# Kernel optimization log

Hardware: AMD Instinct MI355X
Metric: run time of the kernel (lower is better)

## Reference

```python
import jax, jax.numpy as jnp
import numpy as np

NUM_EXPERT = 16
IN_FEAT = 1024
OUT_FEAT = 2048
N_TOKENS = 4096


def setup_inputs() -> dict:
    key = jax.random.key(0)
    k1, k2, k3 = jax.random.split(key, 3)
    x = jax.random.uniform(k1, (N_TOKENS, IN_FEAT), dtype=jnp.float32)
    gate = jax.random.randint(k2, (N_TOKENS,), 0, NUM_EXPERT, dtype=jnp.int32)
    # expert weights: [num_expert, out_feat, in_feat]
    weight = jax.random.normal(k3, (NUM_EXPERT, OUT_FEAT, IN_FEAT), dtype=jnp.float32) * 0.02
    return {"x": x, "gate": gate, "weight": weight}


def reference(x, gate, weight):
    # out[b] = weight[gate[b]] @ x[b]
    # Avoid materializing weight[gate] ([B, O, I] would be huge): scan over the
    # small, fixed expert axis with input masking (tokens not routed to expert e
    # contribute zero rows to that expert's GEMM).
    B = x.shape[0]
    E, O, I = weight.shape
    out0 = jnp.zeros((B, O), dtype=x.dtype)

    def body(out, ew):
        e, W = ew  # W: [O, I]
        xm = jnp.where((gate == e)[:, None], x, 0.0)  # [B, I] masked tokens
        return out + jnp.einsum("bi,oi->bo", xm, W), None

    out, _ = jax.lax.scan(body, out0, (jnp.arange(E), weight))
    return out
```

## Files before the change

### kernel.cpp

```cpp
#include <hip/hip_runtime.h>
#include <hip/hip_bf16.h>
#include <stdint.h>

#define N_TOKENS   4096
#define IN_FEAT    1024
#define OUT_FEAT   2048
#define NUM_EXPERT 16

#define BM 128
#define BN 128
#define BK 32
#define NT (IN_FEAT / BK)
#define MAX_TILES 48
#define MAX_ROWS  6144

typedef __bf16 bf16x8 __attribute__((ext_vector_type(8)));
typedef float  f32x4  __attribute__((ext_vector_type(4)));
typedef unsigned short us8 __attribute__((ext_vector_type(8)));

__device__ __forceinline__ unsigned short f32_to_bf16_rne(float f) {
  union { float f; uint32_t u; } v; v.f = f;
  uint32_t u = v.u;
  u += 0x7fffu + ((u >> 16) & 1u);
  return (unsigned short)(u >> 16);
}

__device__ __forceinline__ void async_copy16(const void* g, void* l) {
  __builtin_amdgcn_global_load_lds(
      (const __attribute__((address_space(1))) unsigned int*)g,
      (__attribute__((address_space(3))) unsigned int*)l, 16, 0, 0);
}

__global__ void k_setup(const int* __restrict__ gate,
                        int* __restrict__ pstart,
                        int* __restrict__ tile_e,
                        int* __restrict__ tile_m,
                        int* __restrict__ row_token)
{
  __shared__ int cnt[NUM_EXPERT];
  __shared__ int cur[NUM_EXPERT];
  __shared__ int ps[NUM_EXPERT];
  const int tid = threadIdx.x;
  if (tid < NUM_EXPERT) { cnt[tid] = 0; cur[tid] = 0; }
  __syncthreads();
  for (int b = tid; b < N_TOKENS; b += 256) atomicAdd(&cnt[gate[b]], 1);
  for (int r = tid; r < MAX_ROWS; r += 256) row_token[r] = -1;
  __syncthreads();
  if (tid == 0) {
    int p = 0, tot = 0;
    for (int e = 0; e < NUM_EXPERT; ++e) {
      ps[e] = p; pstart[e] = p;
      int nt = (cnt[e] + BM - 1) / BM;
      for (int t = 0; t < nt; ++t) { tile_e[tot] = e; tile_m[tot] = t; ++tot; }
      p += nt * BM;
    }
    for (int s = tot; s < MAX_TILES; ++s) { tile_e[s] = -1; tile_m[s] = 0; }
  }
  __syncthreads();
  for (int b = tid; b < N_TOKENS; b += 256) {
    int e = gate[b];
    int pos = atomicAdd(&cur[e], 1);
    row_token[ps[e] + pos] = b;
  }
}

__global__ void k_gather_x(const float4* __restrict__ x,
                           const int* __restrict__ row_token,
                           us8* __restrict__ xs) {
  const int r = blockIdx.x * 2 + (threadIdx.x >> 7);
  const int c = threadIdx.x & 127;
  const int tok = row_token[r];
  us8 o;
  if (tok >= 0) {
    float4 a = x[tok * 256 + c * 2];
    float4 b = x[tok * 256 + c * 2 + 1];
    o[0] = f32_to_bf16_rne(a.x); o[1] = f32_to_bf16_rne(a.y);
    o[2] = f32_to_bf16_rne(a.z); o[3] = f32_to_bf16_rne(a.w);
    o[4] = f32_to_bf16_rne(b.x); o[5] = f32_to_bf16_rne(b.y);
    o[6] = f32_to_bf16_rne(b.z); o[7] = f32_to_bf16_rne(b.w);
  } else {
    o = (us8)0;
  }
  xs[r * 128 + c] = o;
}

__global__ void __launch_bounds__(256, 3)
k_gemm(const unsigned short* __restrict__ xs,
       const float* __restrict__ w,
       const int* __restrict__ pstart,
       const int* __restrict__ tile_e,
       const int* __restrict__ tile_m,
       const int* __restrict__ row_token,
       float* __restrict__ out) {
  __shared__ f32x4 Bs[2][1024];
  __shared__ int rowtok_s[BM];

  const int id  = blockIdx.y * 16 + blockIdx.x;
  const int r_  = id & 7;
  const int m_  = id >> 3;
  const int q3  = m_ % 3;
  const int n_  = m_ / 3;
  const int sub = n_ & 1;
  const int xt  = n_ >> 1;

  const int slot = 2 * (r_ + 8 * q3) + sub;
  const int e = tile_e[slot];
  if (e < 0) return;
  const int seg0 = pstart[e] + tile_m[slot] * BM;
  const int n0 = xt * BN;

  const int tid  = threadIdx.x;
  const int wid  = tid >> 6;
  const int lane = tid & 63;
  const int lr   = lane & 15;
  const int quad = lane >> 4;
  const int wm   = (wid >> 1) * 64;
  const int wn   = (wid & 1) * 64;

  if (tid < BM) rowtok_s[tid] = row_token[seg0 + tid];

  const int cB = (tid & 7) ^ ((tid >> 3) & 7);
  const float* bgp = w + (size_t)e * OUT_FEAT * IN_FEAT
                       + (size_t)(n0 + (tid >> 3)) * IN_FEAT + cB * 4;

  const unsigned short* ap =
      xs + (size_t)(seg0 + wm + lr) * IN_FEAT + quad * 8;

  f32x4 acc[4][4];
  const f32x4 z = {0.f, 0.f, 0.f, 0.f};
#pragma unroll
  for (int i = 0; i < 4; ++i)
#pragma unroll
    for (int j = 0; j < 4; ++j) acc[i][j] = z;

  auto stageB = [&](int t, int b) {
    const int k0 = t * BK;
    async_copy16(bgp + k0,                 Bs[b] + wid * 64);
    async_copy16(bgp + 32 * IN_FEAT + k0,  Bs[b] + 256 + wid * 64);
    async_copy16(bgp + 64 * IN_FEAT + k0,  Bs[b] + 512 + wid * 64);
    async_copy16(bgp + 96 * IN_FEAT + k0,  Bs[b] + 768 + wid * 64);
  };
  auto loadA = [&](int t, bf16x8* dst) {
#pragma unroll
    for (int mi = 0; mi < 4; ++mi)
      dst[mi] = *(const bf16x8*)(ap + (size_t)mi * 16 * IN_FEAT + t * BK);
  };

  bf16x8 afA[4], afB[4];

  stageB(0, 0);
  loadA(0, afA);

  asm volatile("s_waitcnt lgkmcnt(0)" ::: "memory");
  __builtin_amdgcn_s_barrier();

  auto step = [&](int t, bf16x8* afc, bf16x8* afn) {
    const int buf = t & 1;
    if (t + 1 < NT) {
      stageB(t + 1, buf ^ 1);
      loadA(t + 1, afn);
      asm volatile("s_waitcnt vmcnt(8)" ::: "memory");
    } else {
      asm volatile("s_waitcnt vmcnt(0)" ::: "memory");
    }
    __builtin_amdgcn_s_barrier();
    asm volatile("" ::: "memory");

    bf16x8 bf[4];
#pragma unroll
    for (int ni = 0; ni < 4; ++ni) {
      const int n = wn + ni * 16 + lr;
      f32x4 c0 = Bs[buf][n * 8 + ((2 * quad)     ^ (n & 7))];
      f32x4 c1 = Bs[buf][n * 8 + ((2 * quad + 1) ^ (n & 7))];
      bf16x8 b;
      b[0] = (__bf16)c0[0]; b[1] = (__bf16)c0[1];
      b[2] = (__bf16)c0[2]; b[3] = (__bf16)c0[3];
      b[4] = (__bf16)c1[0]; b[5] = (__bf16)c1[1];
      b[6] = (__bf16)c1[2]; b[7] = (__bf16)c1[3];
      bf[ni] = b;
    }
#pragma unroll
    for (int mi = 0; mi < 4; ++mi)
#pragma unroll
      for (int ni = 0; ni < 4; ++ni)
        acc[mi][ni] = __builtin_amdgcn_mfma_f32_16x16x32_bf16(
            afc[mi], bf[ni], acc[mi][ni], 0, 0, 0);

    asm volatile("" ::: "memory");
    __builtin_amdgcn_s_barrier();
  };

  for (int t = 0; t < NT; t += 2) {
    step(t,     afA, afB);
    step(t + 1, afB, afA);
  }

#pragma unroll
  for (int mi = 0; mi < 4; ++mi) {
    const int mb = wm + mi * 16 + quad * 4;
    const int t0 = rowtok_s[mb + 0];
    const int t1 = rowtok_s[mb + 1];
    const int t2 = rowtok_s[mb + 2];
    const int t3 = rowtok_s[mb + 3];
#pragma unroll
    for (int ni = 0; ni < 4; ++ni) {
      const int n = n0 + wn + ni * 16 + lr;
      f32x4 c = acc[mi][ni];
      if (t0 >= 0) out[(size_t)t0 * OUT_FEAT + n] = c[0];
      if (t1 >= 0) out[(size_t)t1 * OUT_FEAT + n] = c[1];
      if (t2 >= 0) out[(size_t)t2 * OUT_FEAT + n] = c[2];
      if (t3 >= 0) out[(size_t)t3 * OUT_FEAT + n] = c[3];
    }
  }
}

extern "C" void kernel_launch(void* const* d_in, const int* in_sizes, int n_in,
                              void* d_out, int out_size, void* d_ws, size_t ws_size,
                              hipStream_t stream) {
  const float* x    = (const float*)d_in[0];
  const int*   gate = (const int*)d_in[1];
  const float* w    = (const float*)d_in[2];
  float* out = (float*)d_out;

  char* ws = (char*)d_ws;
  unsigned short* xs = (unsigned short*)ws;
  int* row_token = (int*)(ws + 12582912);
  int* pstart = row_token + MAX_ROWS;
  int* tile_e = pstart + NUM_EXPERT;
  int* tile_m = tile_e + MAX_TILES;

  k_setup<<<1, 256, 0, stream>>>(gate, pstart, tile_e, tile_m, row_token);
  k_gather_x<<<MAX_ROWS / 2, 256, 0, stream>>>((const float4*)x, row_token,
                                               (us8*)xs);
  dim3 g(OUT_FEAT / BN, MAX_TILES);
  k_gemm<<<g, 256, 0, stream>>>(xs, w, pstart, tile_e, tile_m, row_token, out);
}
```

Measured before the change: 274.9 us.

## Assign one block per expert and N-window, looping over 512-row groups

Replaces the per-M-tile grid with a grid of (expert, 128-column window). Each 512-thread block covers up to 512 rows of an expert's segment per group, so each staged weight tile is reused across four times as many rows. The goal is to cut redundant fp32 weight loads from HBM, which dominate traffic. In exchange the grid shrinks to 256 blocks and per-wave accumulators double, which raises register pressure. Experts with more than 512 rows run the whole K loop again and reload the weights.

Result: faster. 260.4 us (-5.3%).

```diff
diff --git a/kernel.cpp b/kernel.cpp
--- a/kernel.cpp
+++ b/kernel.cpp
@@ -8,10 +8,10 @@
 #define NUM_EXPERT 16
 
 #define BM 128
-#define BN 128
 #define BK 32
 #define NT (IN_FEAT / BK)
-#define MAX_TILES 48
+#define BNW 128
+#define GROWS 512
 #define MAX_ROWS  6144
 
 typedef __bf16 bf16x8 __attribute__((ext_vector_type(8)));
@@ -33,8 +33,6 @@
 
 __global__ void k_setup(const int* __restrict__ gate,
                         int* __restrict__ pstart,
-                        int* __restrict__ tile_e,
-                        int* __restrict__ tile_m,
                         int* __restrict__ row_token)
 {
   __shared__ int cnt[NUM_EXPERT];
@@ -47,14 +45,12 @@
   for (int r = tid; r < MAX_ROWS; r += 256) row_token[r] = -1;
   __syncthreads();
   if (tid == 0) {
-    int p = 0, tot = 0;
+    int p = 0;
     for (int e = 0; e < NUM_EXPERT; ++e) {
       ps[e] = p; pstart[e] = p;
-      int nt = (cnt[e] + BM - 1) / BM;
-      for (int t = 0; t < nt; ++t) { tile_e[tot] = e; tile_m[tot] = t; ++tot; }
-      p += nt * BM;
-    }
-    for (int s = tot; s < MAX_TILES; ++s) { tile_e[s] = -1; tile_m[s] = 0; }
+      p += ((cnt[e] + BM - 1) / BM) * BM;
+    }
+    pstart[NUM_EXPERT] = p;
   }
   __syncthreads();
   for (int b = tid; b < N_TOKENS; b += 256) {
@@ -84,132 +80,134 @@
   xs[r * 128 + c] = o;
 }
 
-__global__ void __launch_bounds__(256, 3)
+__global__ void __launch_bounds__(512, 2)
 k_gemm(const unsigned short* __restrict__ xs,
        const float* __restrict__ w,
        const int* __restrict__ pstart,
-       const int* __restrict__ tile_e,
-       const int* __restrict__ tile_m,
        const int* __restrict__ row_token,
        float* __restrict__ out) {
   __shared__ f32x4 Bs[2][1024];
-  __shared__ int rowtok_s[BM];
-
-  const int id  = blockIdx.y * 16 + blockIdx.x;
-  const int r_  = id & 7;
-  const int m_  = id >> 3;
-  const int q3  = m_ % 3;
-  const int n_  = m_ / 3;
-  const int sub = n_ & 1;
-  const int xt  = n_ >> 1;
-
-  const int slot = 2 * (r_ + 8 * q3) + sub;
-  const int e = tile_e[slot];
-  if (e < 0) return;
-  const int seg0 = pstart[e] + tile_m[slot] * BM;
-  const int n0 = xt * BN;
+  __shared__ int rowtok_s[GROWS];
+
+  const int e    = blockIdx.x;
+  const int nwin = blockIdx.y * BNW;
+  const int seg0 = pstart[e];
+  const int seg_len = pstart[e + 1] - seg0;
+  if (seg_len <= 0) return;
 
   const int tid  = threadIdx.x;
   const int wid  = tid >> 6;
   const int lane = tid & 63;
   const int lr   = lane & 15;
   const int quad = lane >> 4;
-  const int wm   = (wid >> 1) * 64;
-  const int wn   = (wid & 1) * 64;
-
-  if (tid < BM) rowtok_s[tid] = row_token[seg0 + tid];
-
-  const int cB = (tid & 7) ^ ((tid >> 3) & 7);
+
+  const int rB = tid >> 3;
+  const int cB = (tid & 7) ^ (rB & 7);
   const float* bgp = w + (size_t)e * OUT_FEAT * IN_FEAT
-                       + (size_t)(n0 + (tid >> 3)) * IN_FEAT + cB * 4;
-
-  const unsigned short* ap =
-      xs + (size_t)(seg0 + wm + lr) * IN_FEAT + quad * 8;
-
-  f32x4 acc[4][4];
-  const f32x4 z = {0.f, 0.f, 0.f, 0.f};
-#pragma unroll
-  for (int i = 0; i < 4; ++i)
-#pragma unroll
-    for (int j = 0; j < 4; ++j) acc[i][j] = z;
+                       + (size_t)(nwin + rB) * IN_FEAT + cB * 4;
 
   auto stageB = [&](int t, int b) {
     const int k0 = t * BK;
-    async_copy16(bgp + k0,                 Bs[b] + wid * 64);
-    async_copy16(bgp + 32 * IN_FEAT + k0,  Bs[b] + 256 + wid * 64);
-    async_copy16(bgp + 64 * IN_FEAT + k0,  Bs[b] + 512 + wid * 64);
-    async_copy16(bgp + 96 * IN_FEAT + k0,  Bs[b] + 768 + wid * 64);
+    async_copy16(bgp + k0,                Bs[b] +       wid * 64);
+    async_copy16(bgp + 64 * IN_FEAT + k0, Bs[b] + 512 + wid * 64);
   };
-  auto loadA = [&](int t, bf16x8* dst) {
-#pragma unroll
-    for (int mi = 0; mi < 4; ++mi)
-      dst[mi] = *(const bf16x8*)(ap + (size_t)mi * 16 * IN_FEAT + t * BK);
-  };
-
-  bf16x8 afA[4], afB[4];
-
-  stageB(0, 0);
-  loadA(0, afA);
-
-  asm volatile("s_waitcnt lgkmcnt(0)" ::: "memory");
-  __builtin_amdgcn_s_barrier();
-
-  auto step = [&](int t, bf16x8* afc, bf16x8* afn) {
-    const int buf = t & 1;
-    if (t + 1 < NT) {
-      stageB(t + 1, buf ^ 1);
-      loadA(t + 1, afn);
-      asm volatile("s_waitcnt vmcnt(8)" ::: "memory");
-    } else {
-      asm volatile("s_waitcnt vmcnt(0)" ::: "memory");
-    }
+
+  const int nGroups = (seg_len + GROWS - 1) / GROWS;
+
+  for (int g = 0; g < nGroups; ++g) {
+    __syncthreads();
+
+    {
+      const int grow = g * GROWS + tid;
+      rowtok_s[tid] = (grow < seg_len) ? row_token[seg0 + grow] : -1;
+    }
+
+    const unsigned short* apm[4];
+#pragma unroll
+    for (int mi = 0; mi < 4; ++mi) {
+      const int grow = g * GROWS + wid * 64 + mi * 16 + lr;
+      const int arow = (grow < seg_len) ? grow : 0;
+      apm[mi] = xs + (size_t)(seg0 + arow) * IN_FEAT + quad * 8;
+    }
+
+    auto loadA = [&](int t, bf16x8* dst) {
+#pragma unroll
+      for (int mi = 0; mi < 4; ++mi)
+        dst[mi] = *(const bf16x8*)(apm[mi] + t * BK);
+    };
+
+    f32x4 acc[4][8];
+    const f32x4 z = {0.f, 0.f, 0.f, 0.f};
+#pragma unroll
+    for (int i = 0; i < 4; ++i)
+#pragma unroll
+      for (int j = 0; j < 8; ++j) acc[i][j] = z;
+
+    bf16x8 afA[4], afB[4];
+
+    stageB(0, 0);
+    loadA(0, afA);
+
+    asm volatile("s_waitcnt lgkmcnt(0)" ::: "memory");
     __builtin_amdgcn_s_barrier();
-    asm volatile("" ::: "memory");
-
-    bf16x8 bf[4];
-#pragma unroll
-    for (int ni = 0; ni < 4; ++ni) {
-      const int n = wn + ni * 16 + lr;
-      f32x4 c0 = Bs[buf][n * 8 + ((2 * quad)     ^ (n & 7))];
-      f32x4 c1 = Bs[buf][n * 8 + ((2 * quad + 1) ^ (n & 7))];
-      bf16x8 b;
-      b[0] = (__bf16)c0[0]; b[1] = (__bf16)c0[1];
-      b[2] = (__bf16)c0[2]; b[3] = (__bf16)c0[3];
-      b[4] = (__bf16)c1[0]; b[5] = (__bf16)c1[1];
-      b[6] = (__bf16)c1[2]; b[7] = (__bf16)c1[3];
-      bf[ni] = b;
-    }
-#pragma unroll
-    for (int mi = 0; mi < 4; ++mi)
-#pragma unroll
-      for (int ni = 0; ni < 4; ++ni)
-        acc[mi][ni] = __builtin_amdgcn_mfma_f32_16x16x32_bf16(
-            afc[mi], bf[ni], acc[mi][ni], 0, 0, 0);
-
-    asm volatile("" ::: "memory");
-    __builtin_amdgcn_s_barrier();
-  };
-
-  for (int t = 0; t < NT; t += 2) {
-    step(t,     afA, afB);
-    step(t + 1, afB, afA);
-  }
-
-#pragma unroll
-  for (int mi = 0; mi < 4; ++mi) {
-    const int mb = wm + mi * 16 + quad * 4;
-    const int t0 = rowtok_s[mb + 0];
-    const int t1 = rowtok_s[mb + 1];
-    const int t2 = rowtok_s[mb + 2];
-    const int t3 = rowtok_s[mb + 3];
-#pragma unroll
-    for (int ni = 0; ni < 4; ++ni) {
-      const int n = n0 + wn + ni * 16 + lr;
-      f32x4 c = acc[mi][ni];
-      if (t0 >= 0) out[(size_t)t0 * OUT_FEAT + n] = c[0];
-      if (t1 >= 0) out[(size_t)t1 * OUT_FEAT + n] = c[1];
-      if (t2 >= 0) out[(size_t)t2 * OUT_FEAT + n] = c[2];
-      if (t3 >= 0) out[(size_t)t3 * OUT_FEAT + n] = c[3];
+
+    auto step = [&](int t, bf16x8* afc, bf16x8* afn) {
+      const int buf = t & 1;
+      if (t + 1 < NT) {
+        stageB(t + 1, buf ^ 1);
+        loadA(t + 1, afn);
+        asm volatile("s_waitcnt vmcnt(6)" ::: "memory");
+      } else {
+        asm volatile("s_waitcnt vmcnt(0)" ::: "memory");
+      }
+      __builtin_amdgcn_s_barrier();
+      asm volatile("" ::: "memory");
+
+      bf16x8 bf[8];
+#pragma unroll
+      for (int ni = 0; ni < 8; ++ni) {
+        const int n = ni * 16 + lr;
+        f32x4 c0 = Bs[buf][n * 8 + ((2 * quad)     ^ (n & 7))];
+        f32x4 c1 = Bs[buf][n * 8 + ((2 * quad + 1) ^ (n & 7))];
+        bf16x8 b;
+        b[0] = (__bf16)c0[0]; b[1] = (__bf16)c0[1];
+        b[2] = (__bf16)c0[2]; b[3] = (__bf16)c0[3];
+        b[4] = (__bf16)c1[0]; b[5] = (__bf16)c1[1];
+        b[6] = (__bf16)c1[2]; b[7] = (__bf16)c1[3];
+        bf[ni] = b;
+      }
+#pragma unroll
+      for (int mi = 0; mi < 4; ++mi)
+#pragma unroll
+        for (int ni = 0; ni < 8; ++ni)
+          acc[mi][ni] = __builtin_amdgcn_mfma_f32_16x16x32_bf16(
+              afc[mi], bf[ni], acc[mi][ni], 0, 0, 0);
+
+      asm volatile("" ::: "memory");
+      __builtin_amdgcn_s_barrier();
+    };
+
+    for (int t = 0; t < NT; t += 2) {
+      step(t,     afA, afB);
+      step(t + 1, afB, afA);
+    }
+
+#pragma unroll
+    for (int mi = 0; mi < 4; ++mi) {
+      const int mb = wid * 64 + mi * 16 + quad * 4;
+      const int t0 = rowtok_s[mb + 0];
+      const int t1 = rowtok_s[mb + 1];
+      const int t2 = rowtok_s[mb + 2];
+      const int t3 = rowtok_s[mb + 3];
+#pragma unroll
+      for (int ni = 0; ni < 8; ++ni) {
+        const int n = nwin + ni * 16 + lr;
+        f32x4 c = acc[mi][ni];
+        if (t0 >= 0) out[(size_t)t0 * OUT_FEAT + n] = c[0];
+        if (t1 >= 0) out[(size_t)t1 * OUT_FEAT + n] = c[1];
+        if (t2 >= 0) out[(size_t)t2 * OUT_FEAT + n] = c[2];
+        if (t3 >= 0) out[(size_t)t3 * OUT_FEAT + n] = c[3];
+      }
     }
   }
 }
@@ -226,12 +224,10 @@
   unsigned short* xs = (unsigned short*)ws;
   int* row_token = (int*)(ws + 12582912);
   int* pstart = row_token + MAX_ROWS;
-  int* tile_e = pstart + NUM_EXPERT;
-  int* tile_m = tile_e + MAX_TILES;
-
-  k_setup<<<1, 256, 0, stream>>>(gate, pstart, tile_e, tile_m, row_token);
+
+  k_setup<<<1, 256, 0, stream>>>(gate, pstart, row_token);
   k_gather_x<<<MAX_ROWS / 2, 256, 0, stream>>>((const float4*)x, row_token,
                                                (us8*)xs);
-  dim3 g(OUT_FEAT / BN, MAX_TILES);
-  k_gemm<<<g, 256, 0, stream>>>(xs, w, pstart, tile_e, tile_m, row_token, out);
-}
+  dim3 g(NUM_EXPERT, OUT_FEAT / BNW);
+  k_gemm<<<g, 512, 0, stream>>>(xs, w, pstart, row_token, out);
+}
```
